# Kernel tuning notes

Hardware: AMD Instinct MI355X
Metric: run time of the kernel (lower is better)

The kernel has to match this reference:

```python
import jax, jax.numpy as jnp
import numpy as np

V, D, B, L = 100000, 64, 4096, 200

def setup_inputs() -> dict:
    key = jax.random.key(0)
    ks = jax.random.split(key, 10)
    s = 0.05  # keep activations in a sane range for sigmoid
    return {
        "item_ids": jax.random.randint(ks[0], (B,), 0, V),
        "history": jax.random.randint(ks[1], (B, L), 0, V),
        "hist_len": jax.random.randint(ks[2], (B,), 1, L + 1),
        "emb_table": jax.random.normal(ks[3], (V, D), jnp.float32) * s,
        "aW1": jax.random.normal(ks[4], (3 * D, D), jnp.float32) * s,
        "ab1": jnp.zeros((D,), jnp.float32),
        "aW2": jax.random.normal(ks[5], (D, 1), jnp.float32) * s,
        "ab2": jnp.zeros((1,), jnp.float32),
        "fW1": jax.random.normal(ks[6], (3 * D, 128), jnp.float32) * s,
        "fb1": jnp.zeros((128,), jnp.float32),
        "fW2": jax.random.normal(ks[7], (128, 64), jnp.float32) * s,
        "fb2": jnp.zeros((64,), jnp.float32),
        "fW3": jax.random.normal(ks[8], (64, 1), jnp.float32) * s,
        "fb3": jnp.zeros((1,), jnp.float32),
    }

def reference(item_ids, history, hist_len, emb_table, aW1, ab1, aW2, ab2,
              fW1, fb1, fW2, fb2, fW3, fb3):
    target = emb_table[item_ids]                      # [B, D]
    hist = emb_table[history]                         # [B, L, D]
    # original pads short histories with zero rows -> zero the padded tail
    mask = (jnp.arange(hist.shape[1])[None, :] < hist_len[:, None]).astype(hist.dtype)
    hist = hist * mask[..., None]
    tgt = jnp.broadcast_to(target[:, None, :], hist.shape)     # [B, L, D]
    # attention_fc takes 3*D features: (hist, target, hist*target)
    feat = jnp.concatenate([hist, tgt, hist * tgt], axis=-1)   # [B, L, 3D]
    h = jax.nn.relu(feat @ aW1 + ab1)                 # [B, L, D]
    scores = (h @ aW2 + ab2)[..., 0]                  # [B, L]
    # faithful to original: softmax over full padded length (no length mask)
    w = jax.nn.softmax(scores, axis=1)
    pooled = jnp.einsum('bl,bld->bd', w, hist)        # [B, D]
    comb = jnp.concatenate([target, pooled, pooled - target], axis=-1)  # [B, 3D]
    z = jax.nn.relu(comb @ fW1 + fb1)
    z = jax.nn.relu(z @ fW2 + fb2)
    return jax.nn.sigmoid(z @ fW3 + fb3)              # [B, 1]
```

## Files before the change

kernel.cpp:

```cpp
#include <hip/hip_runtime.h>
#include <hip/hip_bf16.h>

#define NV 100000
#define ND 64
#define NB 4096
#define NL 200

typedef __bf16 bf16_t;
typedef __bf16 bf16x8 __attribute__((ext_vector_type(8)));
typedef float f32x4 __attribute__((ext_vector_type(4)));

#define HSTRIDE 72
#define MT 13

__global__ __launch_bounds__(256)
void din_kernel1(const int* __restrict__ item_ids,
                 const int* __restrict__ history,
                 const int* __restrict__ hist_len,
                 const float* __restrict__ emb,
                 const float* __restrict__ aW1,
                 const float* __restrict__ ab1,
                 const float* __restrict__ aW2,
                 float* __restrict__ comb_ws)
{
    __shared__ __align__(16) bf16_t histA[208 * HSTRIDE];
    __shared__ __align__(16) bf16_t wbT[64 * HSTRIDE];
    __shared__ float tgt[64];
    __shared__ float cb[64];
    __shared__ __align__(16) float scores[208];
    __shared__ float wts[208];
    __shared__ float pp[4 * 64];
    __shared__ float red[8];
    __shared__ float pooled[64];

    const int b   = blockIdx.x;
    const int tid = threadIdx.x;
    const int len = hist_len[b];

    if (tid < 64) tgt[tid] = emb[(long)item_ids[b] * ND + tid];

    {
        const int p     = tid & 3;
        const int lbase = tid >> 2;
        for (int pass = 0; pass < 4; ++pass) {
            int l = pass * 64 + lbase;
            if (l < 208) {
                bf16x8 o0 = (bf16x8)(bf16_t)0.f;
                bf16x8 o1 = (bf16x8)(bf16_t)0.f;
                if (l < NL && l < len) {
                    int idx = history[b * NL + l];
                    const float* src = emb + (long)idx * ND + p * 16;
                    f32x4 a0 = *(const f32x4*)(src);
                    f32x4 a1 = *(const f32x4*)(src + 4);
                    f32x4 a2 = *(const f32x4*)(src + 8);
                    f32x4 a3 = *(const f32x4*)(src + 12);
                    for (int i = 0; i < 4; ++i) {
                        o0[i]     = (bf16_t)a0[i];
                        o0[i + 4] = (bf16_t)a1[i];
                        o1[i]     = (bf16_t)a2[i];
                        o1[i + 4] = (bf16_t)a3[i];
                    }
                }
                bf16_t* dst = &histA[l * HSTRIDE + p * 16];
                *(bf16x8*)(dst)     = o0;
                *(bf16x8*)(dst + 8) = o1;
            }
        }
    }
    __syncthreads();

    {
        const int n  = tid & 63;
        const int kp = tid >> 6;
        float csum = 0.f;
        for (int i = 0; i < 16; ++i) {
            int k = kp * 16 + i;
            float tk = tgt[k];
            float w  = aW1[k * 64 + n] + tk * aW1[(128 + k) * 64 + n];
            wbT[n * HSTRIDE + k] = (bf16_t)w;
            csum += tk * aW1[(64 + k) * 64 + n];
        }
        pp[kp * 64 + n] = csum;
    }
    __syncthreads();
    if (tid < 64) cb[tid] = ab1[tid] + pp[tid] + pp[64 + tid] + pp[128 + tid] + pp[192 + tid];
    __syncthreads();

    {
        const int wave = tid >> 6;
        const int lane = tid & 63;
        const int col  = lane & 15;
        const int quad = lane >> 4;

        bf16x8 bfrag[4][2];
        for (int nt = 0; nt < 4; ++nt)
            for (int kb = 0; kb < 2; ++kb)
                bfrag[nt][kb] = *(const bf16x8*)&wbT[(nt * 16 + col) * HSTRIDE + kb * 32 + quad * 8];
        float cvals[4], a2vals[4];
        for (int nt = 0; nt < 4; ++nt) {
            cvals[nt]  = cb[nt * 16 + col];
            a2vals[nt] = aW2[nt * 16 + col];
        }

        for (int mt = wave; mt < MT; mt += 4) {
            const bf16_t* arow = &histA[(mt * 16 + col) * HSTRIDE + quad * 8];
            bf16x8 af0 = *(const bf16x8*)(arow);
            bf16x8 af1 = *(const bf16x8*)(arow + 32);
            float sc[4] = {0.f, 0.f, 0.f, 0.f};
            for (int nt = 0; nt < 4; ++nt) {
                f32x4 acc = {0.f, 0.f, 0.f, 0.f};
                acc = __builtin_amdgcn_mfma_f32_16x16x32_bf16(af0, bfrag[nt][0], acc, 0, 0, 0);
                acc = __builtin_amdgcn_mfma_f32_16x16x32_bf16(af1, bfrag[nt][1], acc, 0, 0, 0);
                for (int i = 0; i < 4; ++i) {
                    float h = acc[i] + cvals[nt];
                    h = h > 0.f ? h : 0.f;
                    sc[i] += h * a2vals[nt];
                }
            }
            for (int off = 1; off < 16; off <<= 1)
                for (int i = 0; i < 4; ++i)
                    sc[i] += __shfl_xor(sc[i], off, 64);
            if (col == 0) {
                f32x4 outv = {sc[0], sc[1], sc[2], sc[3]};
                *(f32x4*)&scores[mt * 16 + quad * 4] = outv;
            }
        }
    }
    __syncthreads();

    {
        float s = (tid < NL) ? scores[tid] : -1e30f;
        float m = s;
        for (int off = 32; off > 0; off >>= 1) m = fmaxf(m, __shfl_xor(m, off, 64));
        if ((tid & 63) == 0) red[tid >> 6] = m;
        __syncthreads();
        m = fmaxf(fmaxf(red[0], red[1]), fmaxf(red[2], red[3]));
        float e = (tid < NL) ? __expf(s - m) : 0.f;
        float ssum = e;
        for (int off = 32; off > 0; off >>= 1) ssum += __shfl_xor(ssum, off, 64);
        if ((tid & 63) == 0) red[4 + (tid >> 6)] = ssum;
        __syncthreads();
        float tot = red[4] + red[5] + red[6] + red[7];
        if (tid < NL) wts[tid] = e / tot;
    }
    __syncthreads();

    {
        const int wave = tid >> 6, lane = tid & 63;
        float acc = 0.f;
        for (int i = 0; i < 50; ++i) {
            int l = wave * 50 + i;
            float wl = wts[l];
            acc += wl * (float)histA[l * HSTRIDE + lane];
        }
        pp[wave * 64 + lane] = acc;
    }
    __syncthreads();
    if (tid < 64) pooled[tid] = pp[tid] + pp[64 + tid] + pp[128 + tid] + pp[192 + tid];
    __syncthreads();

    if (tid < 192) {
        float v;
        if (tid < 64)       v = tgt[tid];
        else if (tid < 128) v = pooled[tid - 64];
        else                v = pooled[tid - 128] - tgt[tid - 128];
        comb_ws[(long)b * 192 + tid] = v;
    }
}

__global__ __launch_bounds__(256)
void din_kernel2(const float* __restrict__ comb,
                 const float* __restrict__ fW1, const float* __restrict__ fb1,
                 const float* __restrict__ fW2, const float* __restrict__ fb2,
                 const float* __restrict__ fW3, const float* __restrict__ fb3,
                 float* __restrict__ out)
{
    __shared__ float z1s[16 * 130];
    __shared__ float z2s[16 * 66];
    const int tid = threadIdx.x;
    const int r   = tid >> 4;
    const int c   = tid & 15;
    const int row = blockIdx.x * 16 + r;

    float acc[8];
    for (int jj = 0; jj < 8; ++jj) acc[jj] = fb1[c * 8 + jj];
    for (int i = 0; i < 192; ++i) {
        float cm = comb[(long)row * 192 + i];
        const float* wr = fW1 + i * 128 + c * 8;
        f32x4 w0 = *(const f32x4*)(wr);
        f32x4 w1 = *(const f32x4*)(wr + 4);
        for (int jj = 0; jj < 4; ++jj) {
            acc[jj]     += cm * w0[jj];
            acc[jj + 4] += cm * w1[jj];
        }
    }
    for (int jj = 0; jj < 8; ++jj) z1s[r * 130 + c * 8 + jj] = fmaxf(acc[jj], 0.f);
    __syncthreads();

    float a2[4];
    for (int jj = 0; jj < 4; ++jj) a2[jj] = fb2[c * 4 + jj];
    for (int i = 0; i < 128; ++i) {
        float zv = z1s[r * 130 + i];
        f32x4 w = *(const f32x4*)(fW2 + i * 64 + c * 4);
        for (int jj = 0; jj < 4; ++jj) a2[jj] += zv * w[jj];
    }
    for (int jj = 0; jj < 4; ++jj) z2s[r * 66 + c * 4 + jj] = fmaxf(a2[jj], 0.f);
    __syncthreads();

    if (c == 0) {
        float s = fb3[0];
        for (int j = 0; j < 64; ++j) s += z2s[r * 66 + j] * fW3[j];
        out[row] = 1.f / (1.f + __expf(-s));
    }
}

extern "C" void kernel_launch(void* const* d_in, const int* in_sizes, int n_in,
                              void* d_out, int out_size, void* d_ws, size_t ws_size,
                              hipStream_t stream) {
    const int*   item_ids = (const int*)d_in[0];
    const int*   history  = (const int*)d_in[1];
    const int*   hist_len = (const int*)d_in[2];
    const float* emb      = (const float*)d_in[3];
    const float* aW1      = (const float*)d_in[4];
    const float* ab1      = (const float*)d_in[5];
    const float* aW2      = (const float*)d_in[6];
    const float* fW1      = (const float*)d_in[8];
    const float* fb1      = (const float*)d_in[9];
    const float* fW2      = (const float*)d_in[10];
    const float* fb2      = (const float*)d_in[11];
    const float* fW3      = (const float*)d_in[12];
    const float* fb3      = (const float*)d_in[13];

    float* comb = (float*)d_ws;

    din_kernel1<<<NB, 256, 0, stream>>>(item_ids, history, hist_len, emb,
                                        aW1, ab1, aW2, comb);
    din_kernel2<<<NB / 16, 256, 0, stream>>>(comb, fW1, fb1, fW2, fb2, fW3, fb3,
                                             (float*)d_out);
}
```

Baseline: 163.5 us.

## Pre-convert embedding table to bf16 and use XOR-swizzled LDS layout

```diff
diff --git a/kernel.cpp b/kernel.cpp
--- a/kernel.cpp
+++ b/kernel.cpp
@@ -5,26 +5,41 @@
 #define ND 64
 #define NB 4096
 #define NL 200
+#define MT 13
 
 typedef __bf16 bf16_t;
 typedef __bf16 bf16x8 __attribute__((ext_vector_type(8)));
 typedef float f32x4 __attribute__((ext_vector_type(4)));
 
-#define HSTRIDE 72
-#define MT 13
+#define TB_ELEMS ((long)NV * ND)
+
+__global__ __launch_bounds__(256)
+void cvt_kernel(const float* __restrict__ emb, bf16_t* __restrict__ tb)
+{
+    long i = ((long)blockIdx.x * 256 + threadIdx.x) * 8;
+    if (i < TB_ELEMS) {
+        f32x4 a0 = *(const f32x4*)(emb + i);
+        f32x4 a1 = *(const f32x4*)(emb + i + 4);
+        bf16x8 o;
+#pragma unroll
+        for (int j = 0; j < 4; ++j) { o[j] = (bf16_t)a0[j]; o[j + 4] = (bf16_t)a1[j]; }
+        *(bf16x8*)(tb + i) = o;
+    }
+}
 
 __global__ __launch_bounds__(256)
 void din_kernel1(const int* __restrict__ item_ids,
                  const int* __restrict__ history,
                  const int* __restrict__ hist_len,
                  const float* __restrict__ emb,
+                 const bf16_t* __restrict__ tb,
                  const float* __restrict__ aW1,
                  const float* __restrict__ ab1,
                  const float* __restrict__ aW2,
                  float* __restrict__ comb_ws)
 {
-    __shared__ __align__(16) bf16_t histA[208 * HSTRIDE];
-    __shared__ __align__(16) bf16_t wbT[64 * HSTRIDE];
+    __shared__ __align__(16) bf16_t histA[208 * 64];
+    __shared__ __align__(16) bf16_t wbT[64 * 64];
     __shared__ float tgt[64];
     __shared__ float cb[64];
     __shared__ __align__(16) float scores[208];
@@ -40,31 +55,41 @@
     if (tid < 64) tgt[tid] = emb[(long)item_ids[b] * ND + tid];
 
     {
-        const int p     = tid & 3;
-        const int lbase = tid >> 2;
-        for (int pass = 0; pass < 4; ++pass) {
-            int l = pass * 64 + lbase;
-            if (l < 208) {
-                bf16x8 o0 = (bf16x8)(bf16_t)0.f;
-                bf16x8 o1 = (bf16x8)(bf16_t)0.f;
-                if (l < NL && l < len) {
-                    int idx = history[b * NL + l];
-                    const float* src = emb + (long)idx * ND + p * 16;
-                    f32x4 a0 = *(const f32x4*)(src);
-                    f32x4 a1 = *(const f32x4*)(src + 4);
-                    f32x4 a2 = *(const f32x4*)(src + 8);
-                    f32x4 a3 = *(const f32x4*)(src + 12);
-                    for (int i = 0; i < 4; ++i) {
-                        o0[i]     = (bf16_t)a0[i];
-                        o0[i + 4] = (bf16_t)a1[i];
-                        o1[i]     = (bf16_t)a2[i];
-                        o1[i + 4] = (bf16_t)a3[i];
-                    }
-                }
-                bf16_t* dst = &histA[l * HSTRIDE + p * 16];
-                *(bf16x8*)(dst)     = o0;
-                *(bf16x8*)(dst + 8) = o1;
-            }
+        const int p  = tid & 1;
+        const int l0 = tid >> 1;
+        const int l1 = l0 + 128;
+        const bf16x8 z = (bf16x8)(bf16_t)0.f;
+        bf16x8 v00 = z, v01 = z, v02 = z, v03 = z;
+        bf16x8 v10 = z, v11 = z, v12 = z, v13 = z;
+        if (l0 < len) {
+            const bf16_t* s = tb + (long)history[(long)b * NL + l0] * ND + p * 32;
+            v00 = *(const bf16x8*)(s);
+            v01 = *(const bf16x8*)(s + 8);
+            v02 = *(const bf16x8*)(s + 16);
+            v03 = *(const bf16x8*)(s + 24);
+        }
+        if (l1 < len) {
+            const bf16_t* s = tb + (long)history[(long)b * NL + l1] * ND + p * 32;
+            v10 = *(const bf16x8*)(s);
+            v11 = *(const bf16x8*)(s + 8);
+            v12 = *(const bf16x8*)(s + 16);
+            v13 = *(const bf16x8*)(s + 24);
+        }
+        {
+            bf16_t* d = &histA[l0 * 64];
+            const int S = (l0 & 7) << 3;
+            *(bf16x8*)&d[(p * 32 +  0) ^ S] = v00;
+            *(bf16x8*)&d[(p * 32 +  8) ^ S] = v01;
+            *(bf16x8*)&d[(p * 32 + 16) ^ S] = v02;
+            *(bf16x8*)&d[(p * 32 + 24) ^ S] = v03;
+        }
+        if (l1 < 208) {
+            bf16_t* d = &histA[l1 * 64];
+            const int S = (l1 & 7) << 3;
+            *(bf16x8*)&d[(p * 32 +  0) ^ S] = v10;
+            *(bf16x8*)&d[(p * 32 +  8) ^ S] = v11;
+            *(bf16x8*)&d[(p * 32 + 16) ^ S] = v12;
+            *(bf16x8*)&d[(p * 32 + 24) ^ S] = v13;
         }
     }
     __syncthreads();
@@ -73,13 +98,18 @@
         const int n  = tid & 63;
         const int kp = tid >> 6;
         float csum = 0.f;
+        bf16x8 w0, w1;
+#pragma unroll
         for (int i = 0; i < 16; ++i) {
             int k = kp * 16 + i;
             float tk = tgt[k];
             float w  = aW1[k * 64 + n] + tk * aW1[(128 + k) * 64 + n];
-            wbT[n * HSTRIDE + k] = (bf16_t)w;
+            if (i < 8) w0[i] = (bf16_t)w; else w1[i - 8] = (bf16_t)w;
             csum += tk * aW1[(64 + k) * 64 + n];
         }
+        const int S = (n & 7) << 3;
+        *(bf16x8*)&wbT[n * 64 + ((kp * 16    ) ^ S)] = w0;
+        *(bf16x8*)&wbT[n * 64 + ((kp * 16 + 8) ^ S)] = w1;
         pp[kp * 64 + n] = csum;
     }
     __syncthreads();
@@ -93,24 +123,34 @@
         const int quad = lane >> 4;
 
         bf16x8 bfrag[4][2];
-        for (int nt = 0; nt < 4; ++nt)
+#pragma unroll
+        for (int nt = 0; nt < 4; ++nt) {
+            const int n = nt * 16 + col;
+            const int S = (n & 7) << 3;
+#pragma unroll
             for (int kb = 0; kb < 2; ++kb)
-                bfrag[nt][kb] = *(const bf16x8*)&wbT[(nt * 16 + col) * HSTRIDE + kb * 32 + quad * 8];
+                bfrag[nt][kb] = *(const bf16x8*)&wbT[n * 64 + ((kb * 32 + quad * 8) ^ S)];
+        }
         float cvals[4], a2vals[4];
+#pragma unroll
         for (int nt = 0; nt < 4; ++nt) {
             cvals[nt]  = cb[nt * 16 + col];
             a2vals[nt] = aW2[nt * 16 + col];
         }
 
         for (int mt = wave; mt < MT; mt += 4) {
-            const bf16_t* arow = &histA[(mt * 16 + col) * HSTRIDE + quad * 8];
-            bf16x8 af0 = *(const bf16x8*)(arow);
-            bf16x8 af1 = *(const bf16x8*)(arow + 32);
+            const int row = mt * 16 + col;
+            const int S   = (row & 7) << 3;
+            const bf16_t* base = &histA[row * 64];
+            bf16x8 af0 = *(const bf16x8*)&base[(     quad * 8) ^ S];
+            bf16x8 af1 = *(const bf16x8*)&base[(32 + quad * 8) ^ S];
             float sc[4] = {0.f, 0.f, 0.f, 0.f};
+#pragma unroll
             for (int nt = 0; nt < 4; ++nt) {
                 f32x4 acc = {0.f, 0.f, 0.f, 0.f};
                 acc = __builtin_amdgcn_mfma_f32_16x16x32_bf16(af0, bfrag[nt][0], acc, 0, 0, 0);
                 acc = __builtin_amdgcn_mfma_f32_16x16x32_bf16(af1, bfrag[nt][1], acc, 0, 0, 0);
+#pragma unroll
                 for (int i = 0; i < 4; ++i) {
                     float h = acc[i] + cvals[nt];
                     h = h > 0.f ? h : 0.f;
@@ -118,6 +158,7 @@
                 }
             }
             for (int off = 1; off < 16; off <<= 1)
+#pragma unroll
                 for (int i = 0; i < 4; ++i)
                     sc[i] += __shfl_xor(sc[i], off, 64);
             if (col == 0) {
@@ -151,7 +192,7 @@
         for (int i = 0; i < 50; ++i) {
             int l = wave * 50 + i;
             float wl = wts[l];
-            acc += wl * (float)histA[l * HSTRIDE + lane];
+            acc += wl * (float)histA[l * 64 + (lane ^ ((l & 7) << 3))];
         }
         pp[wave * 64 + lane] = acc;
     }
@@ -231,9 +272,11 @@
     const float* fW3      = (const float*)d_in[12];
     const float* fb3      = (const float*)d_in[13];
 
-    float* comb = (float*)d_ws;
-
-    din_kernel1<<<NB, 256, 0, stream>>>(item_ids, history, hist_len, emb,
+    bf16_t* tb   = (bf16_t*)d_ws;
+    float*  comb = (float*)((char*)d_ws + (size_t)(TB_ELEMS * 2));
+
+    cvt_kernel<<<(int)(TB_ELEMS / 8 / 256 + 1), 256, 0, stream>>>(emb, tb);
+    din_kernel1<<<NB, 256, 0, stream>>>(item_ids, history, hist_len, emb, tb,
                                         aW1, ab1, aW2, comb);
     din_kernel2<<<NB / 16, 256, 0, stream>>>(comb, fW1, fb1, fW2, fb2, fW3, fb3,
                                              (float*)d_out);
```

New measurement: 163.0 us. No clear change (-0.3%).
